# Optimization experiments

Hardware: AMD Instinct MI355X
Metric: run time of the kernel (lower is better)

Reference implementation:

```python
import jax, jax.numpy as jnp
import numpy as np

V, E, H, L = 32000, 512, 1024, 2
B, S = 16, 128


def _gru_cell(x, h, w_ih, w_hh, b_ih, b_hh):
    # PyTorch GRUCell: gates ordered (r, z, n), chunks of size H
    gi = x @ w_ih.T + b_ih            # (B, 3H)
    gh = h @ w_hh.T + b_hh            # (B, 3H)
    i_r, i_z, i_n = jnp.split(gi, 3, axis=-1)
    h_r, h_z, h_n = jnp.split(gh, 3, axis=-1)
    r = jax.nn.sigmoid(i_r + h_r)
    z = jax.nn.sigmoid(i_z + h_z)
    n = jnp.tanh(i_n + r * h_n)
    return (1.0 - z) * n + z * h


def setup_inputs() -> dict:
    key = jax.random.key(0)
    ks = jax.random.split(key, 16)
    s = lambda fan: 1.0 / np.sqrt(fan)
    inp = {
        "hidden": jax.random.normal(ks[0], (L, B, H), jnp.float32),
        "trg": jax.random.randint(ks[1], (B, S), 0, V),
        "embedding": jax.random.normal(ks[2], (V, E), jnp.float32) * 0.02,
        # layer 0 GRU (input_size=E)
        "w_ih0": jax.random.uniform(ks[3], (3 * H, E), jnp.float32, -s(H), s(H)),
        "w_hh0": jax.random.uniform(ks[4], (3 * H, H), jnp.float32, -s(H), s(H)),
        "b_ih0": jnp.zeros((3 * H,), jnp.float32),
        "b_hh0": jnp.zeros((3 * H,), jnp.float32),
        # layer 1 GRU (input_size=H)
        "w_ih1": jax.random.uniform(ks[5], (3 * H, H), jnp.float32, -s(H), s(H)),
        "w_hh1": jax.random.uniform(ks[6], (3 * H, H), jnp.float32, -s(H), s(H)),
        "b_ih1": jnp.zeros((3 * H,), jnp.float32),
        "b_hh1": jnp.zeros((3 * H,), jnp.float32),
        # output projection MLP: Linear(H,H) -> ReLU -> Linear(H,E)
        "w1": jax.random.uniform(ks[7], (H, H), jnp.float32, -s(H), s(H)),
        "b1": jnp.zeros((H,), jnp.float32),
        "w2": jax.random.uniform(ks[8], (E, H), jnp.float32, -s(H), s(H)),
        "b2": jnp.zeros((E,), jnp.float32),
        # generator bias (weight tied to embedding)
        "b_gen": jnp.zeros((V,), jnp.float32),
    }
    return inp


def reference(hidden, trg, embedding, w_ih0, w_hh0, b_ih0, b_hh0,
              w_ih1, w_hh1, b_ih1, b_hh1, w1, b1, w2, b2, b_gen):
    def step(h, tok):
        # h: (L, B, H); tok: (B,)
        x = embedding[tok]                                 # (B, E)
        h0 = _gru_cell(x, h[0], w_ih0, w_hh0, b_ih0, b_hh0)
        h1 = _gru_cell(h0, h[1], w_ih1, w_hh1, b_ih1, b_hh1)
        new_h = jnp.stack([h0, h1], axis=0)
        out = jax.nn.relu(h1 @ w1.T + b1) @ w2.T + b2      # (B, E)
        logit = out @ embedding.T + b_gen                  # (B, V) weight-tied
        return new_h, logit

    _, logits = jax.lax.scan(step, hidden, trg.T)          # (S, B, V)
    return jnp.transpose(logits, (1, 0, 2))                # (B, S, V)
```

## Files before the change

### kernel.cpp

```cpp
#include <hip/hip_runtime.h>
#include <math.h>

#define Sn 128
#define Bn 16
#define Hn 1024
#define En 512
#define Vn 32000
#define H3 3072
#define NL0 32
#define NL1 64

typedef _Float16 h16;
typedef __attribute__((ext_vector_type(4))) _Float16 h16x4;
typedef __attribute__((ext_vector_type(8))) _Float16 h16x8;
typedef __attribute__((ext_vector_type(4))) float f32x4;

#define Q_EMB   4096000
#define Q_WIH0  (Q_EMB + 393216)
#define Q_W1    (Q_WIH0 + 262144)
#define Q_W2    (Q_W1 + 131072)
#define Q_WHH0  (Q_W2 + 786432)
#define Q_WIH1  (Q_WHH0 + 786432)
#define Q_WHH1  (Q_WIH1 + 786432)
#define Q_HID   (Q_WHH1 + 8192)
__global__ __launch_bounds__(256) void cvt_all_k(
    const float* __restrict__ emb, const float* __restrict__ wih0,
    const float* __restrict__ w1, const float* __restrict__ w2,
    const float* __restrict__ whh0, const float* __restrict__ wih1,
    const float* __restrict__ whh1, const float* __restrict__ hid,
    h16* __restrict__ E, h16* __restrict__ A, h16* __restrict__ B1,
    h16* __restrict__ B2, h16* __restrict__ D0, h16* __restrict__ D1,
    h16* __restrict__ D2, h16* __restrict__ HD)
{
  int i = blockIdx.x * 256 + threadIdx.x;
  const float* s; h16* d; int o;
  if      (i < Q_EMB)  { s = emb;  d = E;  o = i; }
  else if (i < Q_WIH0) { s = wih0; d = A;  o = i - Q_EMB; }
  else if (i < Q_W1)   { s = w1;   d = B1; o = i - Q_WIH0; }
  else if (i < Q_W2)   { s = w2;   d = B2; o = i - Q_W1; }
  else if (i < Q_WHH0) { s = whh0; d = D0; o = i - Q_W2; }
  else if (i < Q_WIH1) { s = wih1; d = D1; o = i - Q_WHH0; }
  else if (i < Q_WHH1) { s = whh1; d = D2; o = i - Q_WIH1; }
  else                 { s = hid;  d = HD; o = i - Q_WHH1; }
  float4 v = *(const float4*)(s + (size_t)o * 4);
  h16x4 ov = { (h16)v.x, (h16)v.y, (h16)v.z, (h16)v.w };
  *(h16x4*)(d + (size_t)o * 4) = ov;
}

__global__ void embed_k(const int* __restrict__ trg, const float* __restrict__ emb,
                        h16* __restrict__ Xh) {
  int t = blockIdx.x;
  int s = t >> 4, b = t & 15;
  int tok = trg[b * Sn + s];
  const float* src = emb + (size_t)tok * En;
  int e = threadIdx.x * 4;
  float4 v = *(const float4*)(src + e);
  h16x4 o = { (h16)v.x, (h16)v.y, (h16)v.z, (h16)v.w };
  *(h16x4*)(Xh + (size_t)t * En + e) = o;
}

template<int OUT_MODE, bool RELU, bool SWZ>
__global__ __launch_bounds__(256) void gemm_bt(
    const h16* __restrict__ A, const h16* __restrict__ B,
    const float* __restrict__ bias, void* __restrict__ C,
    int M, int N, int K)
{
  __shared__ h16 As[128 * 64];
  __shared__ h16 Bs[128 * 64];
  int tid = threadIdx.x;
  int l = tid & 63, wv = tid >> 6;
  int wr = wv >> 1, wc = wv & 1;

  int work = blockIdx.x;
  if (SWZ) { int q = gridDim.x >> 3; work = (work & 7) * q + (work >> 3); }
  int nMp = M >> 7;
  int brow = (work % nMp) << 7;
  int bcol = (work / nMp) << 7;

  f32x4 acc[4][4];
#pragma unroll
  for (int m = 0; m < 4; ++m)
#pragma unroll
    for (int n = 0; n < 4; ++n) acc[m][n] = (f32x4){0.f, 0.f, 0.f, 0.f};

  int nkt = K >> 6;
  for (int kt = 0; kt < nkt; ++kt) {
    const h16* Ag = A + (size_t)brow * K + kt * 64;
    const h16* Bg = B + (size_t)bcol * K + kt * 64;
#pragma unroll
    for (int c = tid; c < 2048; c += 256) {
      int half = c >> 10;
      int cc = c & 1023;
      int row = cc >> 3, slot = cc & 7;
      const h16* src = (half ? Bg : Ag) + (size_t)row * K + slot * 8;
      uint4 v = *(const uint4*)src;
      h16* dst = (half ? Bs : As) + row * 64 + ((slot ^ (row & 7)) << 3);
      *(uint4*)dst = v;
    }
    __syncthreads();
#pragma unroll
    for (int kk = 0; kk < 2; ++kk) {
      h16x8 af[4], bfr[4];
      int rb = wr * 64 + (l & 15);
      int cb2 = wc * 64 + (l & 15);
      int slot = kk * 4 + (l >> 4);
#pragma unroll
      for (int m = 0; m < 4; ++m) {
        int r = rb + m * 16;
        af[m] = *(const h16x8*)&As[r * 64 + ((slot ^ (r & 7)) << 3)];
      }
#pragma unroll
      for (int n = 0; n < 4; ++n) {
        int r = cb2 + n * 16;
        bfr[n] = *(const h16x8*)&Bs[r * 64 + ((slot ^ (r & 7)) << 3)];
      }
#pragma unroll
      for (int m = 0; m < 4; ++m)
#pragma unroll
        for (int n = 0; n < 4; ++n)
          acc[m][n] = __builtin_amdgcn_mfma_f32_16x16x32_f16(af[m], bfr[n], acc[m][n], 0, 0, 0);
    }
    __syncthreads();
  }

#pragma unroll
  for (int m = 0; m < 4; ++m) {
    int row0 = brow + wr * 64 + m * 16 + ((l >> 4) << 2);
#pragma unroll
    for (int n = 0; n < 4; ++n) {
      int col = bcol + wc * 64 + n * 16 + (l & 15);
      float bv = bias ? bias[col] : 0.f;
#pragma unroll
      for (int i = 0; i < 4; ++i) {
        int row = row0 + i;
        float v = acc[m][n][i] + bv;
        if (RELU) v = fmaxf(v, 0.f);
        if (OUT_MODE == 1) {
          ((h16*)C)[(size_t)row * N + col] = (h16)v;
        } else if (OUT_MODE == 2) {
          int rr = ((row & 15) << 7) + (row >> 4);
          ((float*)C)[(size_t)rr * N + col] = v;
        } else {
          ((float*)C)[(size_t)row * N + col] = v;
        }
      }
    }
  }
}

__global__ __launch_bounds__(256, 1) void gemm_bt256(
    const h16* __restrict__ A, const h16* __restrict__ B,
    const float* __restrict__ bias, float* __restrict__ C,
    int M, int N, int K)
{
  __shared__ h16 As[128 * 64];
  __shared__ h16 Bs[256 * 64];
  int tid = threadIdx.x;
  int l = tid & 63, wv = tid >> 6;
  int wr = wv >> 1, wc = wv & 1;

  int work = blockIdx.x;
  int q = gridDim.x >> 3; work = (work & 7) * q + (work >> 3);
  int nMp = M >> 7;
  int brow = (work % nMp) << 7;
  int bcol = (work / nMp) << 8;

  f32x4 acc[4][8];
#pragma unroll
  for (int m = 0; m < 4; ++m)
#pragma unroll
    for (int n = 0; n < 8; ++n) acc[m][n] = (f32x4){0.f, 0.f, 0.f, 0.f};

  int nkt = K >> 6;
  for (int kt = 0; kt < nkt; ++kt) {
    const h16* Ag = A + (size_t)brow * K + kt * 64;
    const h16* Bg = B + (size_t)bcol * K + kt * 64;
#pragma unroll
    for (int c = tid; c < 3072; c += 256) {
      int isB = (c >= 1024);
      int cc = isB ? (c - 1024) : c;
      int row = cc >> 3, slot = cc & 7;
      const h16* src = (isB ? Bg : Ag) + (size_t)row * K + slot * 8;
      uint4 v = *(const uint4*)src;
      h16* dst = (isB ? Bs : As) + row * 64 + ((slot ^ (row & 7)) << 3);
      *(uint4*)dst = v;
    }
    __syncthreads();
#pragma unroll
    for (int kk = 0; kk < 2; ++kk) {
      h16x8 af[4], bfr[8];
      int rb = wr * 64 + (l & 15);
      int cb2 = wc * 128 + (l & 15);
      int slot = kk * 4 + (l >> 4);
#pragma unroll
      for (int m = 0; m < 4; ++m) {
        int r = rb + m * 16;
        af[m] = *(const h16x8*)&As[r * 64 + ((slot ^ (r & 7)) << 3)];
      }
#pragma unroll
      for (int n = 0; n < 8; ++n) {
        int r = cb2 + n * 16;
        bfr[n] = *(const h16x8*)&Bs[r * 64 + ((slot ^ (r & 7)) << 3)];
      }
#pragma unroll
      for (int m = 0; m < 4; ++m)
#pragma unroll
        for (int n = 0; n < 8; ++n)
          acc[m][n] = __builtin_amdgcn_mfma_f32_16x16x32_f16(af[m], bfr[n], acc[m][n], 0, 0, 0);
    }
    __syncthreads();
  }

#pragma unroll
  for (int m = 0; m < 4; ++m) {
    int row0 = brow + wr * 64 + m * 16 + ((l >> 4) << 2);
#pragma unroll
    for (int n = 0; n < 8; ++n) {
      int col = bcol + wc * 128 + n * 16 + (l & 15);
      float bv = bias[col];
#pragma unroll
      for (int i = 0; i < 4; ++i) {
        int row = row0 + i;
        int rr = ((row & 15) << 7) + (row >> 4);
        C[(size_t)rr * N + col] = acc[m][n][i] + bv;
      }
    }
  }
}

__global__ __launch_bounds__(384, 1) void gru_mfma(
    const float* __restrict__ gi0,
    const float* __restrict__ hidden,
    const h16* __restrict__ hinit16,
    const h16* __restrict__ whh0, const float* __restrict__ bhh0,
    const h16* __restrict__ wih1, const float* __restrict__ bih1,
    const h16* __restrict__ whh1, const float* __restrict__ bhh1,
    h16* __restrict__ h0ring,
    h16* __restrict__ H1A,
    int* __restrict__ flags)
{
  __shared__ float exch[5][256];
  int bid = blockIdx.x;
  int tid = threadIdx.x;
  int w = tid >> 6, l = tid & 63;
  int li = l & 15;
  int ko = (l >> 4) << 3;
  int b0 = (l >> 4) << 2;

  __threadfence();

  int* fL0 = flags;
  int* fL1 = flags + 1024;

  if (bid < NL0) {
    int gate = w >> 1, ch = w & 1;
    int j = bid * 32 + ch * 16 + li;
    h16x8 Bf[32];
    {
      const h16* wp = whh0 + ((size_t)((gate << 10) + j) << 10) + ko;
#pragma unroll
      for (int t = 0; t < 32; ++t) Bf[t] = *(const h16x8*)(wp + t * 32);
    }
    float bR = 0.f, bZ = 0.f, bN = 0.f;
    float hprev[4];
    if (gate == 2) {
      bR = bhh0[j]; bZ = bhh0[1024 + j]; bN = bhh0[2048 + j];
#pragma unroll
      for (int i = 0; i < 4; ++i) hprev[i] = hidden[((b0 + i) << 10) + j];
    }

    for (int s = 0; s < Sn; ++s) {
      if (s > 0) {
        if (w == 0 && l < NL0)
          while (__hip_atomic_load(&fL0[l << 5], __ATOMIC_RELAXED, __HIP_MEMORY_SCOPE_AGENT) < s) {}
        __syncthreads();
        asm volatile("" ::: "memory");
      }
      float gr[4], gz[4], gn[4];
      if (gate == 2) {
        const float* gb = gi0 + ((size_t)s << 4) * H3;
#pragma unroll
        for (int i = 0; i < 4; ++i) {
          const float* g = gb + (size_t)(b0 + i) * H3 + j;
          gr[i] = g[0]; gz[i] = g[1024]; gn[i] = g[2048];
        }
      }
      const h16* hsrc = (s == 0) ? hinit16 : h0ring + (((size_t)(s - 1)) << 14);
      const h16* Ap = hsrc + (li << 10) + ko;
      f32x4 acc = (f32x4){0.f, 0.f, 0.f, 0.f};
#pragma unroll
      for (int t = 0; t < 32; ++t)
        acc = __builtin_amdgcn_mfma_f32_16x16x32_f16(*(const h16x8*)(Ap + t * 32), Bf[t], acc, 0, 0, 0);
      if (w < 4) {
#pragma unroll
        for (int i = 0; i < 4; ++i) exch[w][((b0 + i) << 4) + li] = acc[i];
      }
      __syncthreads();
      if (gate == 2) {
#pragma unroll
        for (int i = 0; i < 4; ++i) {
          int e = ((b0 + i) << 4) + li;
          float r = 1.f / (1.f + expf(-(exch[ch][e] + bR + gr[i])));
          float z = 1.f / (1.f + expf(-(exch[2 + ch][e] + bZ + gz[i])));
          float n = tanhf(gn[i] + r * (acc[i] + bN));
          float out = (1.f - z) * n + z * hprev[i];
          hprev[i] = out;
          h16 hv = (h16)out; unsigned short us; __builtin_memcpy(&us, &hv, 2);
          __hip_atomic_store((unsigned short*)h0ring + (((size_t)s) << 14) + ((b0 + i) << 10) + j,
                             us, __ATOMIC_RELAXED, __HIP_MEMORY_SCOPE_AGENT);
        }
      }
      __syncthreads();
      if (tid == 0)
        __hip_atomic_store(&fL0[bid << 5], s + 1, __ATOMIC_RELAXED, __HIP_MEMORY_SCOPE_AGENT);
    }
  } else {
    int bl = bid - NL0;
    int j = (bl << 4) + li;
    int isHH = (w >= 3);
    int gate = isHH ? (w - 3) : w;
    h16x8 Bf[32];
    {
      const h16* wsrc = isHH ? whh1 : wih1;
      const h16* wp = wsrc + ((size_t)((gate << 10) + j) << 10) + ko;
#pragma unroll
      for (int t = 0; t < 32; ++t) Bf[t] = *(const h16x8*)(wp + t * 32);
    }
    float bIR = 0.f, bIZ = 0.f, bIN = 0.f, bHR = 0.f, bHZ = 0.f, bHN = 0.f;
    float hprev[4];
    if (w == 5) {
      bIR = bih1[j]; bIZ = bih1[1024 + j]; bIN = bih1[2048 + j];
      bHR = bhh1[j]; bHZ = bhh1[1024 + j]; bHN = bhh1[2048 + j];
#pragma unroll
      for (int i = 0; i < 4; ++i) hprev[i] = hidden[16384 + ((b0 + i) << 10) + j];
    }

    for (int s = 1; s <= Sn; ++s) {
      if (w == 0) {
        if (l < NL0)
          while (__hip_atomic_load(&fL0[l << 5], __ATOMIC_RELAXED, __HIP_MEMORY_SCOPE_AGENT) < s) {}
      } else if (w == 1 && s >= 2) {
        while (__hip_atomic_load(&fL1[l << 5], __ATOMIC_RELAXED, __HIP_MEMORY_SCOPE_AGENT) < s) {}
      }
      __syncthreads();
      asm volatile("" ::: "memory");
      const h16* hsrc = isHH
          ? ((s == 1) ? hinit16 + 16384 : H1A + (((size_t)(s - 2)) << 14))
          : (h0ring + (((size_t)(s - 1)) << 14));
      const h16* Ap = hsrc + (li << 10) + ko;
      f32x4 acc = (f32x4){0.f, 0.f, 0.f, 0.f};
#pragma unroll
      for (int t = 0; t < 32; ++t)
        acc = __builtin_amdgcn_mfma_f32_16x16x32_f16(*(const h16x8*)(Ap + t * 32), Bf[t], acc, 0, 0, 0);
      if (w < 5) {
#pragma unroll
        for (int i = 0; i < 4; ++i) exch[w][((b0 + i) << 4) + li] = acc[i];
      }
      __syncthreads();
      if (w == 5) {
#pragma unroll
        for (int i = 0; i < 4; ++i) {
          int e = ((b0 + i) << 4) + li;
          float r = 1.f / (1.f + expf(-(exch[0][e] + bIR + exch[3][e] + bHR)));
          float z = 1.f / (1.f + expf(-(exch[1][e] + bIZ + exch[4][e] + bHZ)));
          float n = tanhf(exch[2][e] + bIN + r * (acc[i] + bHN));
          float out = (1.f - z) * n + z * hprev[i];
          hprev[i] = out;
          h16 hv = (h16)out; unsigned short us; __builtin_memcpy(&us, &hv, 2);
          __hip_atomic_store((unsigned short*)H1A + (((size_t)(s - 1)) << 14) + ((b0 + i) << 10) + j,
                             us, __ATOMIC_RELAXED, __HIP_MEMORY_SCOPE_AGENT);
        }
      }
      __syncthreads();
      if (tid == 0)
        __hip_atomic_store(&fL1[bl << 5], s + 1, __ATOMIC_RELAXED, __HIP_MEMORY_SCOPE_AGENT);
    }
  }
}

extern "C" void kernel_launch(void* const* d_in, const int* in_sizes, int n_in,
                              void* d_out, int out_size, void* d_ws, size_t ws_size,
                              hipStream_t stream) {
  const float* hidden = (const float*)d_in[0];
  const int*   trg    = (const int*)d_in[1];
  const float* emb    = (const float*)d_in[2];
  const float* w_ih0  = (const float*)d_in[3];
  const float* w_hh0  = (const float*)d_in[4];
  const float* b_ih0  = (const float*)d_in[5];
  const float* b_hh0  = (const float*)d_in[6];
  const float* w_ih1  = (const float*)d_in[7];
  const float* w_hh1  = (const float*)d_in[8];
  const float* b_ih1  = (const float*)d_in[9];
  const float* b_hh1  = (const float*)d_in[10];
  const float* w1     = (const float*)d_in[11];
  const float* b1     = (const float*)d_in[12];
  const float* w2     = (const float*)d_in[13];
  const float* b2     = (const float*)d_in[14];
  const float* b_gen  = (const float*)d_in[15];

  char* ws = (char*)d_ws;
  size_t off = 0;
  float* GI0    = (float*)(ws + off); off += (size_t)Sn * Bn * H3 * 4;
  h16* Xh       = (h16*)(ws + off);   off += (size_t)Sn * Bn * En * 2;
  h16* embH     = (h16*)(ws + off);   off += (size_t)Vn * En * 2;
  h16* wih0H    = (h16*)(ws + off);   off += (size_t)H3 * En * 2;
  h16* w1H      = (h16*)(ws + off);   off += (size_t)Hn * Hn * 2;
  h16* w2H      = (h16*)(ws + off);   off += (size_t)En * Hn * 2;
  h16* whh0H    = (h16*)(ws + off);   off += (size_t)H3 * Hn * 2;
  h16* wih1H    = (h16*)(ws + off);   off += (size_t)H3 * Hn * 2;
  h16* whh1H    = (h16*)(ws + off);   off += (size_t)H3 * Hn * 2;
  h16* H1A      = (h16*)(ws + off);   off += (size_t)Sn * Bn * Hn * 2;
  h16* h0ring   = (h16*)(ws + off);   off += (size_t)Sn * Bn * Hn * 2;
  h16* hinit16  = (h16*)(ws + off);   off += (size_t)2 * Bn * Hn * 2;
  int* flags    = (int*)(ws + off);   off += 16384;
  h16* Tb = (h16*)GI0;
  h16* Ub = (h16*)((char*)GI0 + (8u << 20));

  cvt_all_k<<<28320, 256, 0, stream>>>(emb, w_ih0, w1, w2, w_hh0, w_ih1, w_hh1, hidden,
                                       embH, wih0H, w1H, w2H, whh0H, wih1H, whh1H, hinit16);
  embed_k<<<Sn * Bn, 128, 0, stream>>>(trg, emb, Xh);

  gemm_bt<0, false, true><<<384, 256, 0, stream>>>(Xh, wih0H, b_ih0, GI0, Sn * Bn, H3, En);

  (void)hipMemsetAsync(flags, 0, 16384, stream);
  gru_mfma<<<NL0 + NL1, 384, 0, stream>>>(GI0, hidden, hinit16,
                                          whh0H, b_hh0, wih1H, b_ih1, whh1H, b_hh1,
                                          h0ring, H1A, flags);

  gemm_bt<1, true,  true><<<128,  256, 0, stream>>>(H1A, w1H, b1, Tb, Sn * Bn, Hn, Hn);
  gemm_bt<1, false, true><<<64,   256, 0, stream>>>(Tb, w2H, b2, Ub, Sn * Bn, En, Hn);
  gemm_bt256<<<2000, 256, 0, stream>>>(Ub, embH, b_gen, (float*)d_out, Sn * Bn, Vn, En);
}
```

Measured before the change: 1.488 ms.

## Replace flag-based GRU step sync with sentinel-poisoned dataflow loads

Removes the per-step flag polling and trailing barrier in the persistent GRU kernel. The hidden-state ring buffers are instead pre-filled with 0xFF (fp16 NaN sentinels), and each wave spins on its own 64-bit atomic loads until no lane holds the sentinel pattern, so consumers start as soon as their specific data lands. Loads are double-buffered in groups of eight and interleaved with two MFMA accumulators, and the LDS exchange buffer is ping-ponged by step parity to stand in for the dropped barrier. This relies on a produced fp16 value never equalling 0xFFFF, adds a large memset, and reads each value with many relaxed atomic loads.

```diff
diff --git a/kernel.cpp b/kernel.cpp
--- a/kernel.cpp
+++ b/kernel.cpp
@@ -14,6 +14,7 @@
 typedef __attribute__((ext_vector_type(4))) _Float16 h16x4;
 typedef __attribute__((ext_vector_type(8))) _Float16 h16x8;
 typedef __attribute__((ext_vector_type(4))) float f32x4;
+typedef unsigned long long u64;
 
 #define Q_EMB   4096000
 #define Q_WIH0  (Q_EMB + 393216)
@@ -228,7 +229,44 @@
   }
 }
 
-__global__ __launch_bounds__(384, 1) void gru_mfma(
+__device__ __forceinline__ bool bad64(u64 x) {
+  u64 m = ~x;
+  return ((m - 0x0001000100010001ull) & ~m & 0x8000800080008000ull) != 0ull;
+}
+__device__ __forceinline__ u64 aload(const u64* p) {
+  return __hip_atomic_load(p, __ATOMIC_RELAXED, __HIP_MEMORY_SCOPE_AGENT);
+}
+
+#define ISSUE8(va, p, t0)                                            \
+  _Pragma("unroll")                                                  \
+  for (int t = 0; t < 8; ++t) {                                      \
+    (va)[2 * t]     = aload((p) + ((t0) + t) * 8);                   \
+    (va)[2 * t + 1] = aload((p) + ((t0) + t) * 8 + 1);               \
+  }
+
+#define CLEAN8(va, p, t0)                                            \
+  for (;;) {                                                         \
+    bool dirty = false;                                              \
+    _Pragma("unroll")                                                \
+    for (int t = 0; t < 8; ++t) {                                    \
+      if (bad64((va)[2 * t]))     { (va)[2 * t]     = aload((p) + ((t0) + t) * 8);     dirty = true; } \
+      if (bad64((va)[2 * t + 1])) { (va)[2 * t + 1] = aload((p) + ((t0) + t) * 8 + 1); dirty = true; } \
+    }                                                                \
+    if (!dirty) break;                                               \
+  }                                                                  \
+  asm volatile("" ::: "memory");
+
+#define MFMA8(a0, a1, va, Bf, t0)                                    \
+  _Pragma("unroll")                                                  \
+  for (int t = 0; t < 8; t += 2) {                                   \
+    union { u64 u[2]; h16x8 v; } A0, A1;                             \
+    A0.u[0] = (va)[2 * t];     A0.u[1] = (va)[2 * t + 1];            \
+    A1.u[0] = (va)[2 * t + 2]; A1.u[1] = (va)[2 * t + 3];            \
+    a0 = __builtin_amdgcn_mfma_f32_16x16x32_f16(A0.v, (Bf)[(t0) + t],     a0, 0, 0, 0); \
+    a1 = __builtin_amdgcn_mfma_f32_16x16x32_f16(A1.v, (Bf)[(t0) + t + 1], a1, 0, 0, 0); \
+  }
+
+__global__ __launch_bounds__(384, 2) void gru_df(
     const float* __restrict__ gi0,
     const float* __restrict__ hidden,
     const h16* __restrict__ hinit16,
@@ -236,21 +274,16 @@
     const h16* __restrict__ wih1, const float* __restrict__ bih1,
     const h16* __restrict__ whh1, const float* __restrict__ bhh1,
     h16* __restrict__ h0ring,
-    h16* __restrict__ H1A,
-    int* __restrict__ flags)
+    h16* __restrict__ H1A)
 {
-  __shared__ float exch[5][256];
+  __shared__ float exch[2][5][256];
   int bid = blockIdx.x;
   int tid = threadIdx.x;
   int w = tid >> 6, l = tid & 63;
   int li = l & 15;
   int ko = (l >> 4) << 3;
   int b0 = (l >> 4) << 2;
-
-  __threadfence();
-
-  int* fL0 = flags;
-  int* fL1 = flags + 1024;
+  int u64b = ((li << 10) + ko) >> 2;
 
   if (bid < NL0) {
     int gate = w >> 1, ch = w & 1;
@@ -270,12 +303,6 @@
     }
 
     for (int s = 0; s < Sn; ++s) {
-      if (s > 0) {
-        if (w == 0 && l < NL0)
-          while (__hip_atomic_load(&fL0[l << 5], __ATOMIC_RELAXED, __HIP_MEMORY_SCOPE_AGENT) < s) {}
-        __syncthreads();
-        asm volatile("" ::: "memory");
-      }
       float gr[4], gz[4], gn[4];
       if (gate == 2) {
         const float* gb = gi0 + ((size_t)s << 4) * H3;
@@ -286,22 +313,35 @@
         }
       }
       const h16* hsrc = (s == 0) ? hinit16 : h0ring + (((size_t)(s - 1)) << 14);
-      const h16* Ap = hsrc + (li << 10) + ko;
-      f32x4 acc = (f32x4){0.f, 0.f, 0.f, 0.f};
-#pragma unroll
-      for (int t = 0; t < 32; ++t)
-        acc = __builtin_amdgcn_mfma_f32_16x16x32_f16(*(const h16x8*)(Ap + t * 32), Bf[t], acc, 0, 0, 0);
+      const u64* p = (const u64*)hsrc + u64b;
+      u64 va[2][16];
+      f32x4 a0 = (f32x4){0.f, 0.f, 0.f, 0.f};
+      f32x4 a1 = (f32x4){0.f, 0.f, 0.f, 0.f};
+      ISSUE8(va[0], p, 0)
+      ISSUE8(va[1], p, 8)
+      CLEAN8(va[0], p, 0)
+      MFMA8(a0, a1, va[0], Bf, 0)
+      ISSUE8(va[0], p, 16)
+      CLEAN8(va[1], p, 8)
+      MFMA8(a0, a1, va[1], Bf, 8)
+      ISSUE8(va[1], p, 24)
+      CLEAN8(va[0], p, 16)
+      MFMA8(a0, a1, va[0], Bf, 16)
+      CLEAN8(va[1], p, 24)
+      MFMA8(a0, a1, va[1], Bf, 24)
+      f32x4 acc = a0 + a1;
+      int pb = s & 1;
       if (w < 4) {
 #pragma unroll
-        for (int i = 0; i < 4; ++i) exch[w][((b0 + i) << 4) + li] = acc[i];
+        for (int i = 0; i < 4; ++i) exch[pb][w][((b0 + i) << 4) + li] = acc[i];
       }
       __syncthreads();
       if (gate == 2) {
 #pragma unroll
         for (int i = 0; i < 4; ++i) {
           int e = ((b0 + i) << 4) + li;
-          float r = 1.f / (1.f + expf(-(exch[ch][e] + bR + gr[i])));
-          float z = 1.f / (1.f + expf(-(exch[2 + ch][e] + bZ + gz[i])));
+          float r = 1.f / (1.f + expf(-(exch[pb][ch][e] + bR + gr[i])));
+          float z = 1.f / (1.f + expf(-(exch[pb][2 + ch][e] + bZ + gz[i])));
           float n = tanhf(gn[i] + r * (acc[i] + bN));
           float out = (1.f - z) * n + z * hprev[i];
           hprev[i] = out;
@@ -310,9 +350,6 @@
                              us, __ATOMIC_RELAXED, __HIP_MEMORY_SCOPE_AGENT);
         }
       }
-      __syncthreads();
-      if (tid == 0)
-        __hip_atomic_store(&fL0[bid << 5], s + 1, __ATOMIC_RELAXED, __HIP_MEMORY_SCOPE_AGENT);
     }
   } else {
     int bl = bid - NL0;
@@ -336,34 +373,39 @@
     }
 
     for (int s = 1; s <= Sn; ++s) {
-      if (w == 0) {
-        if (l < NL0)
-          while (__hip_atomic_load(&fL0[l << 5], __ATOMIC_RELAXED, __HIP_MEMORY_SCOPE_AGENT) < s) {}
-      } else if (w == 1 && s >= 2) {
-        while (__hip_atomic_load(&fL1[l << 5], __ATOMIC_RELAXED, __HIP_MEMORY_SCOPE_AGENT) < s) {}
-      }
-      __syncthreads();
-      asm volatile("" ::: "memory");
       const h16* hsrc = isHH
           ? ((s == 1) ? hinit16 + 16384 : H1A + (((size_t)(s - 2)) << 14))
           : (h0ring + (((size_t)(s - 1)) << 14));
-      const h16* Ap = hsrc + (li << 10) + ko;
-      f32x4 acc = (f32x4){0.f, 0.f, 0.f, 0.f};
-#pragma unroll
-      for (int t = 0; t < 32; ++t)
-        acc = __builtin_amdgcn_mfma_f32_16x16x32_f16(*(const h16x8*)(Ap + t * 32), Bf[t], acc, 0, 0, 0);
+      const u64* p = (const u64*)hsrc + u64b;
+      u64 va[2][16];
+      f32x4 a0 = (f32x4){0.f, 0.f, 0.f, 0.f};
+      f32x4 a1 = (f32x4){0.f, 0.f, 0.f, 0.f};
+      ISSUE8(va[0], p, 0)
+      ISSUE8(va[1], p, 8)
+      CLEAN8(va[0], p, 0)
+      MFMA8(a0, a1, va[0], Bf, 0)
+      ISSUE8(va[0], p, 16)
+      CLEAN8(va[1], p, 8)
+      MFMA8(a0, a1, va[1], Bf, 8)
+      ISSUE8(va[1], p, 24)
+      CLEAN8(va[0], p, 16)
+      MFMA8(a0, a1, va[0], Bf, 16)
+      CLEAN8(va[1], p, 24)
+      MFMA8(a0, a1, va[1], Bf, 24)
+      f32x4 acc = a0 + a1;
+      int pb = s & 1;
       if (w < 5) {
 #pragma unroll
-        for (int i = 0; i < 4; ++i) exch[w][((b0 + i) << 4) + li] = acc[i];
+        for (int i = 0; i < 4; ++i) exch[pb][w][((b0 + i) << 4) + li] = acc[i];
       }
       __syncthreads();
       if (w == 5) {
 #pragma unroll
         for (int i = 0; i < 4; ++i) {
           int e = ((b0 + i) << 4) + li;
-          float r = 1.f / (1.f + expf(-(exch[0][e] + bIR + exch[3][e] + bHR)));
-          float z = 1.f / (1.f + expf(-(exch[1][e] + bIZ + exch[4][e] + bHZ)));
-          float n = tanhf(exch[2][e] + bIN + r * (acc[i] + bHN));
+          float r = 1.f / (1.f + expf(-(exch[pb][0][e] + bIR + exch[pb][3][e] + bHR)));
+          float z = 1.f / (1.f + expf(-(exch[pb][1][e] + bIZ + exch[pb][4][e] + bHZ)));
+          float n = tanhf(exch[pb][2][e] + bIN + r * (acc[i] + bHN));
           float out = (1.f - z) * n + z * hprev[i];
           hprev[i] = out;
           h16 hv = (h16)out; unsigned short us; __builtin_memcpy(&us, &hv, 2);
@@ -371,9 +413,6 @@
                              us, __ATOMIC_RELAXED, __HIP_MEMORY_SCOPE_AGENT);
         }
       }
-      __syncthreads();
-      if (tid == 0)
-        __hip_atomic_store(&fL1[bl << 5], s + 1, __ATOMIC_RELAXED, __HIP_MEMORY_SCOPE_AGENT);
     }
   }
 }
@@ -412,7 +451,6 @@
   h16* H1A      = (h16*)(ws + off);   off += (size_t)Sn * Bn * Hn * 2;
   h16* h0ring   = (h16*)(ws + off);   off += (size_t)Sn * Bn * Hn * 2;
   h16* hinit16  = (h16*)(ws + off);   off += (size_t)2 * Bn * Hn * 2;
-  int* flags    = (int*)(ws + off);   off += 16384;
   h16* Tb = (h16*)GI0;
   h16* Ub = (h16*)((char*)GI0 + (8u << 20));
 
@@ -422,10 +460,10 @@
 
   gemm_bt<0, false, true><<<384, 256, 0, stream>>>(Xh, wih0H, b_ih0, GI0, Sn * Bn, H3, En);
 
-  (void)hipMemsetAsync(flags, 0, 16384, stream);
-  gru_mfma<<<NL0 + NL1, 384, 0, stream>>>(GI0, hidden, hinit16,
-                                          whh0H, b_hh0, wih1H, b_ih1, whh1H, b_hh1,
-                                          h0ring, H1A, flags);
+  (void)hipMemsetAsync(H1A, 0xFF, (size_t)2 * Sn * Bn * Hn * 2, stream);
+  gru_df<<<NL0 + NL1, 384, 0, stream>>>(GI0, hidden, hinit16,
+                                        whh0H, b_hh0, wih1H, b_ih1, whh1H, b_hh1,
+                                        h0ring, H1A);
 
   gemm_bt<1, true,  true><<<128,  256, 0, stream>>>(H1A, w1H, b1, Tb, Sn * Bn, Hn, Hn);
   gemm_bt<1, false, true><<<64,   256, 0, stream>>>(Tb, w2H, b2, Ub, Sn * Bn, En, Hn);
```

New measurement: 3.679 ms. +147.1%, slower.

## Pin GRU blocks by XCD and replace block barriers with per-wave flag polling

Applied to the files above, without the earlier changes.

Launches 256 blocks and keeps only those with blockIdx mod 8 in {0,1,2}. The intent is to place the layer-0 and layer-1 persistent GRU blocks on chosen XCDs so that blocks which share flags and hidden state sit closer together. The per-step spin-then-syncthreads is replaced by every wave polling packed flags itself, with per-wave flag stores after an explicit vmcnt wait, and the exchange buffer is double-buffered so one barrier per step is dropped. The recurrent MFMA chain is split into two accumulators with staged A-fragment loads to hide latency. This relies on the hardware dispatching blocks round-robin across XCDs and on relaxed atomics giving correct ordering, and it adds extra polling traffic.

```diff
diff --git a/kernel.cpp b/kernel.cpp
--- a/kernel.cpp
+++ b/kernel.cpp
@@ -7,8 +7,6 @@
 #define En 512
 #define Vn 32000
 #define H3 3072
-#define NL0 32
-#define NL1 64
 
 typedef _Float16 h16;
 typedef __attribute__((ext_vector_type(4))) _Float16 h16x4;
@@ -228,7 +226,18 @@
   }
 }
 
-__global__ __launch_bounds__(384, 1) void gru_mfma(
+#define LOADG(dst, base, t0)                                           \
+  _Pragma("unroll")                                                    \
+  for (int t = 0; t < 8; ++t) (dst)[t] = *(const h16x8*)((base) + ((t0) + t) * 32);
+
+#define CHAING(a0, a1, src, Bw, t0)                                    \
+  _Pragma("unroll")                                                    \
+  for (int t = 0; t < 8; t += 2) {                                     \
+    a0 = __builtin_amdgcn_mfma_f32_16x16x32_f16((src)[t],     (Bw)[(t0) + t],     a0, 0, 0, 0); \
+    a1 = __builtin_amdgcn_mfma_f32_16x16x32_f16((src)[t + 1], (Bw)[(t0) + t + 1], a1, 0, 0, 0); \
+  }
+
+__global__ __launch_bounds__(384) void gru_pin(
     const float* __restrict__ gi0,
     const float* __restrict__ hidden,
     const h16* __restrict__ hinit16,
@@ -239,8 +248,10 @@
     h16* __restrict__ H1A,
     int* __restrict__ flags)
 {
-  __shared__ float exch[5][256];
+  __shared__ float exch[2][5][256];
   int bid = blockIdx.x;
+  int res = bid & 7;
+  if (res > 2) return;
   int tid = threadIdx.x;
   int w = tid >> 6, l = tid & 63;
   int li = l & 15;
@@ -252,14 +263,17 @@
   int* fL0 = flags;
   int* fL1 = flags + 1024;
 
-  if (bid < NL0) {
+  if (res == 0) {
+    int blk = bid >> 3;
     int gate = w >> 1, ch = w & 1;
-    int j = bid * 32 + ch * 16 + li;
+    int j = blk * 32 + ch * 16 + li;
     h16x8 Bf[32];
     {
       const h16* wp = whh0 + ((size_t)((gate << 10) + j) << 10) + ko;
 #pragma unroll
       for (int t = 0; t < 32; ++t) Bf[t] = *(const h16x8*)(wp + t * 32);
+#pragma unroll
+      for (int t = 0; t < 32; ++t) asm volatile("" : "+v"(Bf[t]));
     }
     float bR = 0.f, bZ = 0.f, bN = 0.f;
     float hprev[4];
@@ -270,12 +284,6 @@
     }
 
     for (int s = 0; s < Sn; ++s) {
-      if (s > 0) {
-        if (w == 0 && l < NL0)
-          while (__hip_atomic_load(&fL0[l << 5], __ATOMIC_RELAXED, __HIP_MEMORY_SCOPE_AGENT) < s) {}
-        __syncthreads();
-        asm volatile("" ::: "memory");
-      }
       float gr[4], gz[4], gn[4];
       if (gate == 2) {
         const float* gb = gi0 + ((size_t)s << 4) * H3;
@@ -285,23 +293,36 @@
           gr[i] = g[0]; gz[i] = g[1024]; gn[i] = g[2048];
         }
       }
+      asm volatile("" ::: "memory");
+      if (s > 0) {
+        while (__hip_atomic_load(&fL0[l], __ATOMIC_RELAXED, __HIP_MEMORY_SCOPE_AGENT) < s) {}
+        asm volatile("" ::: "memory");
+      }
       const h16* hsrc = (s == 0) ? hinit16 : h0ring + (((size_t)(s - 1)) << 14);
       const h16* Ap = hsrc + (li << 10) + ko;
-      f32x4 acc = (f32x4){0.f, 0.f, 0.f, 0.f};
-#pragma unroll
-      for (int t = 0; t < 32; ++t)
-        acc = __builtin_amdgcn_mfma_f32_16x16x32_f16(*(const h16x8*)(Ap + t * 32), Bf[t], acc, 0, 0, 0);
+      h16x8 va[8], vb[8];
+      f32x4 a0 = (f32x4){0.f, 0.f, 0.f, 0.f};
+      f32x4 a1 = (f32x4){0.f, 0.f, 0.f, 0.f};
+      LOADG(va, Ap, 0)  LOADG(vb, Ap, 8)
+      CHAING(a0, a1, va, Bf, 0)
+      LOADG(va, Ap, 16)
+      CHAING(a0, a1, vb, Bf, 8)
+      LOADG(vb, Ap, 24)
+      CHAING(a0, a1, va, Bf, 16)
+      CHAING(a0, a1, vb, Bf, 24)
+      f32x4 acc = a0 + a1;
+      int pb = s & 1;
       if (w < 4) {
 #pragma unroll
-        for (int i = 0; i < 4; ++i) exch[w][((b0 + i) << 4) + li] = acc[i];
+        for (int i = 0; i < 4; ++i) exch[pb][w][((b0 + i) << 4) + li] = acc[i];
       }
       __syncthreads();
       if (gate == 2) {
 #pragma unroll
         for (int i = 0; i < 4; ++i) {
           int e = ((b0 + i) << 4) + li;
-          float r = 1.f / (1.f + expf(-(exch[ch][e] + bR + gr[i])));
-          float z = 1.f / (1.f + expf(-(exch[2 + ch][e] + bZ + gz[i])));
+          float r = 1.f / (1.f + expf(-(exch[pb][ch][e] + bR + gr[i])));
+          float z = 1.f / (1.f + expf(-(exch[pb][2 + ch][e] + bZ + gz[i])));
           float n = tanhf(gn[i] + r * (acc[i] + bN));
           float out = (1.f - z) * n + z * hprev[i];
           hprev[i] = out;
@@ -309,14 +330,14 @@
           __hip_atomic_store((unsigned short*)h0ring + (((size_t)s) << 14) + ((b0 + i) << 10) + j,
                              us, __ATOMIC_RELAXED, __HIP_MEMORY_SCOPE_AGENT);
         }
-      }
-      __syncthreads();
-      if (tid == 0)
-        __hip_atomic_store(&fL0[bid << 5], s + 1, __ATOMIC_RELAXED, __HIP_MEMORY_SCOPE_AGENT);
+        asm volatile("s_waitcnt vmcnt(0)" ::: "memory");
+        if (l == 0)
+          __hip_atomic_store(&fL0[blk * 2 + ch], s + 1, __ATOMIC_RELAXED, __HIP_MEMORY_SCOPE_AGENT);
+      }
     }
   } else {
-    int bl = bid - NL0;
-    int j = (bl << 4) + li;
+    int idx = ((bid >> 3) << 1) + (res - 1);
+    int j = (idx << 4) + li;
     int isHH = (w >= 3);
     int gate = isHH ? (w - 3) : w;
     h16x8 Bf[32];
@@ -325,6 +346,8 @@
       const h16* wp = wsrc + ((size_t)((gate << 10) + j) << 10) + ko;
 #pragma unroll
       for (int t = 0; t < 32; ++t) Bf[t] = *(const h16x8*)(wp + t * 32);
+#pragma unroll
+      for (int t = 0; t < 32; ++t) asm volatile("" : "+v"(Bf[t]));
     }
     float bIR = 0.f, bIZ = 0.f, bIN = 0.f, bHR = 0.f, bHZ = 0.f, bHN = 0.f;
     float hprev[4];
@@ -336,44 +359,52 @@
     }
 
     for (int s = 1; s <= Sn; ++s) {
-      if (w == 0) {
-        if (l < NL0)
-          while (__hip_atomic_load(&fL0[l << 5], __ATOMIC_RELAXED, __HIP_MEMORY_SCOPE_AGENT) < s) {}
-      } else if (w == 1 && s >= 2) {
-        while (__hip_atomic_load(&fL1[l << 5], __ATOMIC_RELAXED, __HIP_MEMORY_SCOPE_AGENT) < s) {}
-      }
-      __syncthreads();
       asm volatile("" ::: "memory");
+      if (!isHH) {
+        while (__hip_atomic_load(&fL0[l], __ATOMIC_RELAXED, __HIP_MEMORY_SCOPE_AGENT) < s) {}
+        asm volatile("" ::: "memory");
+      } else if (s >= 2) {
+        while (__hip_atomic_load(&fL1[l], __ATOMIC_RELAXED, __HIP_MEMORY_SCOPE_AGENT) < s - 1) {}
+        asm volatile("" ::: "memory");
+      }
       const h16* hsrc = isHH
           ? ((s == 1) ? hinit16 + 16384 : H1A + (((size_t)(s - 2)) << 14))
           : (h0ring + (((size_t)(s - 1)) << 14));
       const h16* Ap = hsrc + (li << 10) + ko;
-      f32x4 acc = (f32x4){0.f, 0.f, 0.f, 0.f};
-#pragma unroll
-      for (int t = 0; t < 32; ++t)
-        acc = __builtin_amdgcn_mfma_f32_16x16x32_f16(*(const h16x8*)(Ap + t * 32), Bf[t], acc, 0, 0, 0);
+      h16x8 va[8], vb[8];
+      f32x4 a0 = (f32x4){0.f, 0.f, 0.f, 0.f};
+      f32x4 a1 = (f32x4){0.f, 0.f, 0.f, 0.f};
+      LOADG(va, Ap, 0)  LOADG(vb, Ap, 8)
+      CHAING(a0, a1, va, Bf, 0)
+      LOADG(va, Ap, 16)
+      CHAING(a0, a1, vb, Bf, 8)
+      LOADG(vb, Ap, 24)
+      CHAING(a0, a1, va, Bf, 16)
+      CHAING(a0, a1, vb, Bf, 24)
+      f32x4 acc = a0 + a1;
+      int pb = s & 1;
       if (w < 5) {
 #pragma unroll
-        for (int i = 0; i < 4; ++i) exch[w][((b0 + i) << 4) + li] = acc[i];
+        for (int i = 0; i < 4; ++i) exch[pb][w][((b0 + i) << 4) + li] = acc[i];
       }
       __syncthreads();
       if (w == 5) {
 #pragma unroll
         for (int i = 0; i < 4; ++i) {
           int e = ((b0 + i) << 4) + li;
-          float r = 1.f / (1.f + expf(-(exch[0][e] + bIR + exch[3][e] + bHR)));
-          float z = 1.f / (1.f + expf(-(exch[1][e] + bIZ + exch[4][e] + bHZ)));
-          float n = tanhf(exch[2][e] + bIN + r * (acc[i] + bHN));
+          float r = 1.f / (1.f + expf(-(exch[pb][0][e] + bIR + exch[pb][3][e] + bHR)));
+          float z = 1.f / (1.f + expf(-(exch[pb][1][e] + bIZ + exch[pb][4][e] + bHZ)));
+          float n = tanhf(exch[pb][2][e] + bIN + r * (acc[i] + bHN));
           float out = (1.f - z) * n + z * hprev[i];
           hprev[i] = out;
           h16 hv = (h16)out; unsigned short us; __builtin_memcpy(&us, &hv, 2);
           __hip_atomic_store((unsigned short*)H1A + (((size_t)(s - 1)) << 14) + ((b0 + i) << 10) + j,
                              us, __ATOMIC_RELAXED, __HIP_MEMORY_SCOPE_AGENT);
         }
-      }
-      __syncthreads();
-      if (tid == 0)
-        __hip_atomic_store(&fL1[bl << 5], s + 1, __ATOMIC_RELAXED, __HIP_MEMORY_SCOPE_AGENT);
+        asm volatile("s_waitcnt vmcnt(0)" ::: "memory");
+        if (l == 0)
+          __hip_atomic_store(&fL1[idx], s, __ATOMIC_RELAXED, __HIP_MEMORY_SCOPE_AGENT);
+      }
     }
   }
 }
@@ -412,7 +443,7 @@
   h16* H1A      = (h16*)(ws + off);   off += (size_t)Sn * Bn * Hn * 2;
   h16* h0ring   = (h16*)(ws + off);   off += (size_t)Sn * Bn * Hn * 2;
   h16* hinit16  = (h16*)(ws + off);   off += (size_t)2 * Bn * Hn * 2;
-  int* flags    = (int*)(ws + off);   off += 16384;
+  int* flags    = (int*)(ws + off);   off += 32768;
   h16* Tb = (h16*)GI0;
   h16* Ub = (h16*)((char*)GI0 + (8u << 20));
 
@@ -422,10 +453,10 @@
 
   gemm_bt<0, false, true><<<384, 256, 0, stream>>>(Xh, wih0H, b_ih0, GI0, Sn * Bn, H3, En);
 
-  (void)hipMemsetAsync(flags, 0, 16384, stream);
-  gru_mfma<<<NL0 + NL1, 384, 0, stream>>>(GI0, hidden, hinit16,
-                                          whh0H, b_hh0, wih1H, b_ih1, whh1H, b_hh1,
-                                          h0ring, H1A, flags);
+  (void)hipMemsetAsync(flags, 0, 32768, stream);
+  gru_pin<<<256, 384, 0, stream>>>(GI0, hidden, hinit16,
+                                   whh0H, b_hh0, wih1H, b_ih1, whh1H, b_hh1,
+                                   h0ring, H1A, flags);
 
   gemm_bt<1, true,  true><<<128,  256, 0, stream>>>(H1A, w1H, b1, Tb, Sn * Bn, Hn, Hn);
   gemm_bt<1, false, true><<<64,   256, 0, stream>>>(Tb, w2H, b2, Ub, Sn * Bn, En, Hn);
```

New measurement: 2.693 ms. 1.81x slower.

## Pipeline GRU recurrence MFMA chains and use per-wave flag signaling

Applied to the files above, without the earlier changes.

The persistent GRU kernel now splits each 32-step MFMA chain into two interleaved accumulators with software-pipelined A-operand loads. Flag publication moves from a block-wide barrier plus a thread-0 store to a per-wave store after s_waitcnt, and the flag layout is compacted. The gi0 loads are hoisted above the spin-wait, and weight registers are pinned with asm constraints. The goal is to shorten the serial per-step latency of the recurrence, at the cost of more register pressure and looser ordering guarantees (relaxed atomics after vmcnt wait).

```diff
diff --git a/kernel.cpp b/kernel.cpp
--- a/kernel.cpp
+++ b/kernel.cpp
@@ -228,7 +228,36 @@
   }
 }
 
-__global__ __launch_bounds__(384, 1) void gru_mfma(
+#define LOAD4(dst, base, t0)                                           \
+  _Pragma("unroll")                                                    \
+  for (int t = 0; t < 4; ++t) (dst)[t] = *(const h16x8*)((base) + ((t0) + t) * 32);
+
+#define CHAIN4(a0, a1, src, Bw, t0)                                    \
+  _Pragma("unroll")                                                    \
+  for (int t = 0; t < 4; t += 2) {                                     \
+    a0 = __builtin_amdgcn_mfma_f32_16x16x32_f16((src)[t],     (Bw)[(t0) + t],     a0, 0, 0, 0); \
+    a1 = __builtin_amdgcn_mfma_f32_16x16x32_f16((src)[t + 1], (Bw)[(t0) + t + 1], a1, 0, 0, 0); \
+  }
+
+#define PIPE32(a0, a1, Ap, Bf)                                         \
+  {                                                                    \
+    h16x8 va[4], vb[4];                                                \
+    LOAD4(va, Ap, 0)  LOAD4(vb, Ap, 4)                                 \
+    CHAIN4(a0, a1, va, Bf, 0)   LOAD4(va, Ap, 8)                       \
+    CHAIN4(a0, a1, vb, Bf, 4)   LOAD4(vb, Ap, 12)                      \
+    CHAIN4(a0, a1, va, Bf, 8)   LOAD4(va, Ap, 16)                      \
+    CHAIN4(a0, a1, vb, Bf, 12)  LOAD4(vb, Ap, 20)                      \
+    CHAIN4(a0, a1, va, Bf, 16)  LOAD4(va, Ap, 24)                      \
+    CHAIN4(a0, a1, vb, Bf, 20)  LOAD4(vb, Ap, 28)                      \
+    CHAIN4(a0, a1, va, Bf, 24)                                         \
+    CHAIN4(a0, a1, vb, Bf, 28)                                         \
+  }
+
+#define PINW(Bf)                                                       \
+  _Pragma("unroll")                                                    \
+  for (int t = 0; t < 32; ++t) asm volatile("" : "+v"((Bf)[t]));
+
+__global__ __launch_bounds__(384, 2) void gru_pin2(
     const float* __restrict__ gi0,
     const float* __restrict__ hidden,
     const h16* __restrict__ hinit16,
@@ -250,11 +279,12 @@
   __threadfence();
 
   int* fL0 = flags;
-  int* fL1 = flags + 1024;
+  int* fL1 = flags + 512;
 
   if (bid < NL0) {
+    int blk = bid;
     int gate = w >> 1, ch = w & 1;
-    int j = bid * 32 + ch * 16 + li;
+    int j = blk * 32 + ch * 16 + li;
     h16x8 Bf[32];
     {
       const h16* wp = whh0 + ((size_t)((gate << 10) + j) << 10) + ko;
@@ -270,12 +300,7 @@
     }
 
     for (int s = 0; s < Sn; ++s) {
-      if (s > 0) {
-        if (w == 0 && l < NL0)
-          while (__hip_atomic_load(&fL0[l << 5], __ATOMIC_RELAXED, __HIP_MEMORY_SCOPE_AGENT) < s) {}
-        __syncthreads();
-        asm volatile("" ::: "memory");
-      }
+      PINW(Bf)
       float gr[4], gz[4], gn[4];
       if (gate == 2) {
         const float* gb = gi0 + ((size_t)s << 4) * H3;
@@ -285,12 +310,18 @@
           gr[i] = g[0]; gz[i] = g[1024]; gn[i] = g[2048];
         }
       }
+      if (s > 0) {
+        if (w == 0)
+          while (__hip_atomic_load(&fL0[l << 2], __ATOMIC_RELAXED, __HIP_MEMORY_SCOPE_AGENT) < s) {}
+        __syncthreads();
+        asm volatile("" ::: "memory");
+      }
       const h16* hsrc = (s == 0) ? hinit16 : h0ring + (((size_t)(s - 1)) << 14);
       const h16* Ap = hsrc + (li << 10) + ko;
-      f32x4 acc = (f32x4){0.f, 0.f, 0.f, 0.f};
-#pragma unroll
-      for (int t = 0; t < 32; ++t)
-        acc = __builtin_amdgcn_mfma_f32_16x16x32_f16(*(const h16x8*)(Ap + t * 32), Bf[t], acc, 0, 0, 0);
+      f32x4 a0 = (f32x4){0.f, 0.f, 0.f, 0.f};
+      f32x4 a1 = (f32x4){0.f, 0.f, 0.f, 0.f};
+      PIPE32(a0, a1, Ap, Bf)
+      f32x4 acc = a0 + a1;
       if (w < 4) {
 #pragma unroll
         for (int i = 0; i < 4; ++i) exch[w][((b0 + i) << 4) + li] = acc[i];
@@ -309,14 +340,15 @@
           __hip_atomic_store((unsigned short*)h0ring + (((size_t)s) << 14) + ((b0 + i) << 10) + j,
                              us, __ATOMIC_RELAXED, __HIP_MEMORY_SCOPE_AGENT);
         }
-      }
-      __syncthreads();
-      if (tid == 0)
-        __hip_atomic_store(&fL0[bid << 5], s + 1, __ATOMIC_RELAXED, __HIP_MEMORY_SCOPE_AGENT);
+        asm volatile("s_waitcnt vmcnt(0)" ::: "memory");
+        if (l == 0)
+          __hip_atomic_store(&fL0[(blk * 2 + ch) << 2], s + 1,
+                             __ATOMIC_RELAXED, __HIP_MEMORY_SCOPE_AGENT);
+      }
     }
   } else {
-    int bl = bid - NL0;
-    int j = (bl << 4) + li;
+    int idx = bid - NL0;
+    int j = (idx << 4) + li;
     int isHH = (w >= 3);
     int gate = isHH ? (w - 3) : w;
     h16x8 Bf[32];
@@ -336,11 +368,11 @@
     }
 
     for (int s = 1; s <= Sn; ++s) {
+      PINW(Bf)
       if (w == 0) {
-        if (l < NL0)
-          while (__hip_atomic_load(&fL0[l << 5], __ATOMIC_RELAXED, __HIP_MEMORY_SCOPE_AGENT) < s) {}
+        while (__hip_atomic_load(&fL0[l << 2], __ATOMIC_RELAXED, __HIP_MEMORY_SCOPE_AGENT) < s) {}
       } else if (w == 1 && s >= 2) {
-        while (__hip_atomic_load(&fL1[l << 5], __ATOMIC_RELAXED, __HIP_MEMORY_SCOPE_AGENT) < s) {}
+        while (__hip_atomic_load(&fL1[l << 2], __ATOMIC_RELAXED, __HIP_MEMORY_SCOPE_AGENT) < s - 1) {}
       }
       __syncthreads();
       asm volatile("" ::: "memory");
@@ -348,10 +380,10 @@
           ? ((s == 1) ? hinit16 + 16384 : H1A + (((size_t)(s - 2)) << 14))
           : (h0ring + (((size_t)(s - 1)) << 14));
       const h16* Ap = hsrc + (li << 10) + ko;
-      f32x4 acc = (f32x4){0.f, 0.f, 0.f, 0.f};
-#pragma unroll
-      for (int t = 0; t < 32; ++t)
-        acc = __builtin_amdgcn_mfma_f32_16x16x32_f16(*(const h16x8*)(Ap + t * 32), Bf[t], acc, 0, 0, 0);
+      f32x4 a0 = (f32x4){0.f, 0.f, 0.f, 0.f};
+      f32x4 a1 = (f32x4){0.f, 0.f, 0.f, 0.f};
+      PIPE32(a0, a1, Ap, Bf)
+      f32x4 acc = a0 + a1;
       if (w < 5) {
 #pragma unroll
         for (int i = 0; i < 4; ++i) exch[w][((b0 + i) << 4) + li] = acc[i];
@@ -370,10 +402,10 @@
           __hip_atomic_store((unsigned short*)H1A + (((size_t)(s - 1)) << 14) + ((b0 + i) << 10) + j,
                              us, __ATOMIC_RELAXED, __HIP_MEMORY_SCOPE_AGENT);
         }
-      }
-      __syncthreads();
-      if (tid == 0)
-        __hip_atomic_store(&fL1[bl << 5], s + 1, __ATOMIC_RELAXED, __HIP_MEMORY_SCOPE_AGENT);
+        asm volatile("s_waitcnt vmcnt(0)" ::: "memory");
+        if (l == 0)
+          __hip_atomic_store(&fL1[idx << 2], s, __ATOMIC_RELAXED, __HIP_MEMORY_SCOPE_AGENT);
+      }
     }
   }
 }
@@ -412,7 +444,7 @@
   h16* H1A      = (h16*)(ws + off);   off += (size_t)Sn * Bn * Hn * 2;
   h16* h0ring   = (h16*)(ws + off);   off += (size_t)Sn * Bn * Hn * 2;
   h16* hinit16  = (h16*)(ws + off);   off += (size_t)2 * Bn * Hn * 2;
-  int* flags    = (int*)(ws + off);   off += 16384;
+  int* flags    = (int*)(ws + off);   off += 8192;
   h16* Tb = (h16*)GI0;
   h16* Ub = (h16*)((char*)GI0 + (8u << 20));
 
@@ -422,8 +454,8 @@
 
   gemm_bt<0, false, true><<<384, 256, 0, stream>>>(Xh, wih0H, b_ih0, GI0, Sn * Bn, H3, En);
 
-  (void)hipMemsetAsync(flags, 0, 16384, stream);
-  gru_mfma<<<NL0 + NL1, 384, 0, stream>>>(GI0, hidden, hinit16,
+  (void)hipMemsetAsync(flags, 0, 8192, stream);
+  gru_pin2<<<NL0 + NL1, 384, 0, stream>>>(GI0, hidden, hinit16,
                                           whh0H, b_hh0, wih1H, b_ih1, whh1H, b_hh1,
                                           h0ring, H1A, flags);
 
```

After: 1.637 ms. +10.0%, slower.
